# Kernel optimization log

Measured on AMD Instinct MI355X. Metric: run time of the kernel, lower is better.

Reference implementation:

```python
import jax, jax.numpy as jnp
import numpy as np
from jax import lax

# --- config matching init_kwargs ---
VOXEL_SIZE = np.array([0.25, 0.25, 8.0], np.float32)
PC_RANGE = np.array([-50.0, -50.0, -5.0, 50.0, 50.0, 3.0], np.float32)
MAX_PTS = 32
MAX_VOX = 60000
GRID = np.round((PC_RANGE[3:] - PC_RANGE[:3]) / VOXEL_SIZE).astype(np.int64)  # [400,400,1] (x,y,z)
GX, GY, GZ = int(GRID[0]), int(GRID[1]), int(GRID[2])
BIG = GX * GY * GZ  # sentinel flat id for out-of-range points
N_POINTS = 1_200_000
N_FEATS = 5


def voxelize(points):
    """points: [N, 3+C] float. Returns (out_voxels [V,P,3+C], out_coords [V,3] zyx, out_num_points [V])."""
    N = points.shape[0]
    vsize = jnp.asarray(VOXEL_SIZE)
    vmin = jnp.asarray(PC_RANGE[:3])
    # integer voxel coords per point (x,y,z)
    cxyz = jnp.floor((points[:, :3] - vmin) / vsize).astype(jnp.int32)  # [N,3]
    grid = jnp.asarray(GRID, jnp.int32)
    in_range = jnp.all((cxyz >= 0) & (cxyz < grid), axis=-1)  # [N]
    flat = cxyz[:, 2] * (GY * GX) + cxyz[:, 1] * GX + cxyz[:, 0]
    flat = jnp.where(in_range, flat, BIG)
    # stable sort by voxel id: points within a voxel keep original order (like CPU fill order)
    order = jnp.argsort(flat, stable=True)
    sf = flat[order]                      # sorted flat ids, invalid (BIG) at end
    sp = points[order]                    # [N, D]
    sc = cxyz[order]                      # [N, 3]
    ar = jnp.arange(N, dtype=jnp.int32)
    valid = sf < BIG
    new_seg = jnp.concatenate([jnp.ones((1,), bool), sf[1:] != sf[:-1]])
    first = valid & new_seg               # first point of each non-empty voxel
    vox_idx = jnp.cumsum(first.astype(jnp.int32)) - 1          # voxel slot per point
    seg_start = lax.associative_scan(jnp.maximum, jnp.where(first, ar, 0))
    rank = ar - seg_start                 # position of point within its voxel
    keep = valid & (vox_idx < MAX_VOX) & (rank < MAX_PTS)
    # out-of-bound index MAX_VOX + mode='drop' discards non-kept points
    sv = jnp.where(keep, vox_idx, MAX_VOX)
    sr = jnp.where(keep, rank, 0)
    D = points.shape[1]
    out_voxels = jnp.zeros((MAX_VOX, MAX_PTS, D), points.dtype).at[sv, sr].set(sp, mode='drop')
    out_num_points = jnp.zeros((MAX_VOX,), jnp.int32).at[sv].add(
        keep.astype(jnp.int32), mode='drop')
    coords_zyx = sc[:, ::-1]              # reorder to [z,y,x] as in the torch module
    out_coords = jnp.zeros((MAX_VOX, 3), jnp.int32).at[sv].set(coords_zyx, mode='drop')
    return out_voxels, out_coords, out_num_points


def setup_inputs() -> dict:
    key = jax.random.key(0)
    u = jax.random.uniform(key, (N_POINTS, N_FEATS), jnp.float32)
    # xyz spans slightly beyond the valid range so out-of-range masking is exercised
    lo = jnp.array([-55.0, -55.0, -6.0, 0.0, 0.0], jnp.float32)
    hi = jnp.array([55.0, 55.0, 4.0, 1.0, 1.0], jnp.float32)
    points = lo + u * (hi - lo)
    return {"points": points}


def reference(points):
    return voxelize(points)
```

## Files before the change

### kernel.cpp

```cpp
#include <hip/hip_runtime.h>


constexpr int GXc = 400;
constexpr int GYc = 400;
constexpr int NCELL = GXc * GYc;
constexpr int MAXV  = 60000;
constexpr int MAXP  = 32;
constexpr int NF    = 5;

constexpr int SCAN_B = 256;
constexpr int SCAN_E = 8;
constexpr int SCAN_TILE = SCAN_B * SCAN_E;
constexpr int NSCANBLK = (NCELL + SCAN_TILE - 1) / SCAN_TILE;

__device__ __forceinline__ int point_cell(float x, float y, float z) {
    int cx = (int)floorf((x + 50.0f) * 4.0f);
    int cy = (int)floorf((y + 50.0f) * 4.0f);
    int cz = (int)floorf((z + 5.0f) * 0.125f);
    if (cx < 0 || cx >= GXc || cy < 0 || cy >= GYc || cz != 0) return -1;
    return cy * GXc + cx;
}

__global__ void __launch_bounds__(256)
k_bin(const float* __restrict__ pts, int N,
      unsigned char* __restrict__ occupied, int* __restrict__ cellId) {
    int t = blockIdx.x * blockDim.x + threadIdx.x;
    int i0 = t * 4;
    if (i0 >= N) return;
    if (N - i0 >= 4) {
        const float4* src = (const float4*)(pts + (size_t)i0 * NF);
        float4 q0 = src[0], q1 = src[1], q2 = src[2], q3 = src[3], q4 = src[4];
        float f[20];
        *(float4*)(f + 0)  = q0; *(float4*)(f + 4)  = q1; *(float4*)(f + 8)  = q2;
        *(float4*)(f + 12) = q3; *(float4*)(f + 16) = q4;
        int cs[4];
        #pragma unroll
        for (int k = 0; k < 4; k++)
            cs[k] = point_cell(f[k * 5 + 0], f[k * 5 + 1], f[k * 5 + 2]);
        *(int4*)(cellId + i0) = make_int4(cs[0], cs[1], cs[2], cs[3]);
        #pragma unroll
        for (int k = 0; k < 4; k++)
            if (cs[k] >= 0) occupied[cs[k]] = 1;
    } else {
        for (int k = 0; k < N - i0; k++) {
            const float* p = pts + (size_t)(i0 + k) * NF;
            int c = point_cell(p[0], p[1], p[2]);
            cellId[i0 + k] = c;
            if (c >= 0) occupied[c] = 1;
        }
    }
}

__global__ void k_scanA(const unsigned char* __restrict__ occupied,
                        int* __restrict__ excl, int* __restrict__ blockSums) {
    __shared__ int sh[SCAN_B];
    int base = blockIdx.x * SCAN_TILE;
    int idx0 = base + threadIdx.x * SCAN_E;
    unsigned long long occ8 = 0;
    if (idx0 < NCELL) occ8 = *(const unsigned long long*)(occupied + idx0);
    int vals[SCAN_E];
    int sum = 0;
    #pragma unroll
    for (int e = 0; e < SCAN_E; e++) {
        int v = (int)((occ8 >> (8 * e)) & 1ull);
        vals[e] = sum;
        sum += v;
    }
    sh[threadIdx.x] = sum;
    __syncthreads();
    for (int off = 1; off < SCAN_B; off <<= 1) {
        int t = (threadIdx.x >= (unsigned)off) ? sh[threadIdx.x - off] : 0;
        __syncthreads();
        sh[threadIdx.x] += t;
        __syncthreads();
    }
    int thrExcl = (threadIdx.x == 0) ? 0 : sh[threadIdx.x - 1];
    #pragma unroll
    for (int e = 0; e < SCAN_E; e++) {
        int idx = idx0 + e;
        if (idx < NCELL) excl[idx] = thrExcl + vals[e];
    }
    if (threadIdx.x == SCAN_B - 1) blockSums[blockIdx.x] = sh[SCAN_B - 1];
}

__global__ void k_scanB(const unsigned char* __restrict__ occupied,
                        const int* __restrict__ excl,
                        const int* __restrict__ blockSums,
                        int* __restrict__ voxId,
                        int* __restrict__ cellOfVox,
                        int* __restrict__ nvoxOut) {
    __shared__ int sb[128];
    int tid = threadIdx.x;
    if (tid < 128) sb[tid] = (tid < NSCANBLK) ? blockSums[tid] : 0;
    __syncthreads();
    for (int off = 1; off < 128; off <<= 1) {
        int t = (tid < 128 && tid >= off) ? sb[tid - off] : 0;
        __syncthreads();
        if (tid < 128) sb[tid] += t;
        __syncthreads();
    }
    int c = blockIdx.x * blockDim.x + tid;
    if (c < NCELL) {
        int vi = -1;
        if (occupied[c]) {
            int blk = c / SCAN_TILE;
            int basev = (blk == 0) ? 0 : sb[blk - 1];
            int v = basev + excl[c];
            if (v < MAXV) { vi = v; cellOfVox[v] = c; }
        }
        voxId[c] = vi;
    }
    if (blockIdx.x == 0 && tid == 0) {
        int tot = sb[NSCANBLK - 1];
        *nvoxOut = tot < MAXV ? tot : MAXV;
    }
}

__global__ void __launch_bounds__(256)
k_scatter2(const int* __restrict__ cellId, int N,
           const int* __restrict__ voxId,
           int* __restrict__ vcount, int* __restrict__ slots) {
    int t = blockIdx.x * blockDim.x + threadIdx.x;
    int i0 = t * 4;
    if (i0 >= N) return;
    if (N - i0 >= 4) {
        int4 cc = *(const int4*)(cellId + i0);
        int cs[4] = {cc.x, cc.y, cc.z, cc.w};
        #pragma unroll
        for (int k = 0; k < 4; k++) {
            int c = cs[k];
            if (c >= 0) {
                int v = voxId[c];
                if (v >= 0) {
                    int pos = atomicAdd(&vcount[v], 1);
                    if (pos < MAXP) slots[v * MAXP + pos] = i0 + k;
                }
            }
        }
    } else {
        for (int k = 0; k < N - i0; k++) {
            int c = cellId[i0 + k];
            if (c >= 0) {
                int v = voxId[c];
                if (v >= 0) {
                    int pos = atomicAdd(&vcount[v], 1);
                    if (pos < MAXP) slots[v * MAXP + pos] = i0 + k;
                }
            }
        }
    }
}

__global__ void __launch_bounds__(256)
k_finalize(const float* __restrict__ pts, int N,
           const int* __restrict__ vcount,
           const int* __restrict__ slots,
           const int* __restrict__ cellOfVox,
           const int* __restrict__ nvoxPtr,
           float* __restrict__ outVox,
           float* __restrict__ outCoord,
           float* __restrict__ outNum) {
    constexpr int WV = 4;
    __shared__ float s_dat[WV][MAXP * NF];
    __shared__ int   s_key[WV][MAXP];
    __shared__ int   s_srt[WV][MAXP];

    int wv   = threadIdx.x >> 6;
    int lane = threadIdx.x & 63;
    int v    = blockIdx.x * WV + wv;
    int nvox = *nvoxPtr;

    int c = 0, num = 0;
    bool live = (v < nvox);
    if (live) {
        c = cellOfVox[v];
        int cnt = vcount[v];
        num = cnt < MAXP ? cnt : MAXP;
    }

    if (lane < MAXP)
        s_key[wv][lane] = (live && lane < num) ? slots[v * MAXP + lane] : 0x7fffffff;
    #pragma unroll
    for (int k = 0; k < 3; k++) {
        int idx = lane + 64 * k;
        if (idx < MAXP * NF) s_dat[wv][idx] = 0.0f;
    }
    __syncthreads();

    if (lane < MAXP) {
        int key = s_key[wv][lane];
        int rank = 0;
        #pragma unroll
        for (int j = 0; j < MAXP; j++) rank += (s_key[wv][j] < key) ? 1 : 0;
        if (live && lane < num) s_srt[wv][rank] = key;
    }
    __syncthreads();

    if (live && lane < num) {
        int p = s_srt[wv][lane];
        size_t byte0 = (size_t)p * 20;
        float r0, r1, r2, r3, r4, r5, r6, r7;
        int sel;
        if (byte0 + 32 <= (size_t)N * 20) {
            const float4* f4 = (const float4*)pts;
            size_t w = byte0 >> 4;
            sel = (int)((byte0 & 15) >> 2);
            float4 qa = f4[w], qb = f4[w + 1];
            r0 = qa.x; r1 = qa.y; r2 = qa.z; r3 = qa.w;
            r4 = qb.x; r5 = qb.y; r6 = qb.z; r7 = qb.w;
        } else {
            const float* s = pts + (size_t)p * NF;
            r0 = s[0]; r1 = s[1]; r2 = s[2]; r3 = s[3]; r4 = s[4];
            r5 = r6 = r7 = 0.0f; sel = 0;
        }
        float o0 = sel == 0 ? r0 : sel == 1 ? r1 : sel == 2 ? r2 : r3;
        float o1 = sel == 0 ? r1 : sel == 1 ? r2 : sel == 2 ? r3 : r4;
        float o2 = sel == 0 ? r2 : sel == 1 ? r3 : sel == 2 ? r4 : r5;
        float o3 = sel == 0 ? r3 : sel == 1 ? r4 : sel == 2 ? r5 : r6;
        float o4 = sel == 0 ? r4 : sel == 1 ? r5 : sel == 2 ? r6 : r7;
        float* d = &s_dat[wv][lane * NF];
        d[0] = o0; d[1] = o1; d[2] = o2; d[3] = o3; d[4] = o4;
    }
    __syncthreads();

    const float4* sv = (const float4*)s_dat[wv];
    float4* dst = (float4*)(outVox + (size_t)v * (MAXP * NF));
    if (lane < 40) dst[lane] = sv[lane];
    if (lane == 40) outCoord[(size_t)v * 3 + 0] = 0.0f;
    if (lane == 41) outCoord[(size_t)v * 3 + 1] = live ? (float)(c / GXc) : 0.0f;
    if (lane == 42) outCoord[(size_t)v * 3 + 2] = live ? (float)(c % GXc) : 0.0f;
    if (lane == 43) outNum[v] = live ? (float)num : 0.0f;
}

extern "C" void kernel_launch(void* const* d_in, const int* in_sizes, int n_in,
                              void* d_out, int out_size, void* d_ws, size_t ws_size,
                              hipStream_t stream) {
    const float* pts = (const float*)d_in[0];
    int N = in_sizes[0] / NF;

    float* out      = (float*)d_out;
    float* outVox   = out;
    float* outCoord = out + (size_t)MAXV * MAXP * NF;
    float* outNum   = outCoord + (size_t)MAXV * 3;

    char* ws = (char*)d_ws;
    auto take = [&](size_t bytes) {
        char* p = ws;
        ws += (bytes + 255) & ~(size_t)255;
        return p;
    };
    unsigned char* occupied = (unsigned char*)take((size_t)NCELL);
    int* vcount    = (int*)take((size_t)MAXV * 4);
    int* cellId    = (int*)take((size_t)((N + 3) & ~3) * 4);
    int* excl      = (int*)take((size_t)NCELL * 4);
    int* blockSums = (int*)take((size_t)128 * 4);
    int* voxId     = (int*)take((size_t)NCELL * 4);
    int* cellOfVox = (int*)take((size_t)MAXV * 4);
    int* slots     = (int*)take((size_t)MAXV * MAXP * 4);
    int* nvoxBuf   = (int*)take(256);

    size_t zeroBytes = (size_t)((char*)(vcount + MAXV) - (char*)occupied);
    hipMemsetAsync(occupied, 0, zeroBytes, stream);

    int nt = (N + 3) / 4;
    int nb = (nt + 255) / 256;
    k_bin<<<nb, 256, 0, stream>>>(pts, N, occupied, cellId);
    k_scanA<<<NSCANBLK, SCAN_B, 0, stream>>>(occupied, excl, blockSums);
    k_scanB<<<(NCELL + 255) / 256, 256, 0, stream>>>(occupied, excl, blockSums,
                                                     voxId, cellOfVox, nvoxBuf);
    k_scatter2<<<nb, 256, 0, stream>>>(cellId, N, voxId, vcount, slots);
    k_finalize<<<MAXV / 4, 256, 0, stream>>>(pts, N, vcount, slots, cellOfVox,
                                             nvoxBuf, outVox, outCoord, outNum);
}
```

Baseline: 129.1 us.

## Process 16 voxels per finalize block and 8 points per scatter thread

The finalize kernel now gives each wave four voxels, split into two half-wave groups of 32 lanes with two voxels per lane. This drops the block-wide __syncthreads that were only needed for wave-private shared memory and issues both voxels' point gathers before either is used, so more memory loads are in flight. The scatter kernel handles 8 points per thread and does all voxId lookups before the atomics, again to overlap loads. In exchange, fewer blocks are launched and more registers are used per thread, and correctness now depends on wave-synchronous shared-memory access without barriers.

```diff
diff --git a/kernel.cpp b/kernel.cpp
--- a/kernel.cpp
+++ b/kernel.cpp
@@ -121,20 +121,21 @@
            const int* __restrict__ voxId,
            int* __restrict__ vcount, int* __restrict__ slots) {
     int t = blockIdx.x * blockDim.x + threadIdx.x;
-    int i0 = t * 4;
+    int i0 = t * 8;
     if (i0 >= N) return;
-    if (N - i0 >= 4) {
-        int4 cc = *(const int4*)(cellId + i0);
-        int cs[4] = {cc.x, cc.y, cc.z, cc.w};
+    if (N - i0 >= 8) {
+        int4 a = *(const int4*)(cellId + i0);
+        int4 b = *(const int4*)(cellId + i0 + 4);
+        int cs[8] = {a.x, a.y, a.z, a.w, b.x, b.y, b.z, b.w};
+        int vs[8];
         #pragma unroll
-        for (int k = 0; k < 4; k++) {
-            int c = cs[k];
-            if (c >= 0) {
-                int v = voxId[c];
-                if (v >= 0) {
-                    int pos = atomicAdd(&vcount[v], 1);
-                    if (pos < MAXP) slots[v * MAXP + pos] = i0 + k;
-                }
+        for (int k = 0; k < 8; k++)
+            vs[k] = (cs[k] >= 0) ? voxId[cs[k]] : -1;
+        #pragma unroll
+        for (int k = 0; k < 8; k++) {
+            if (vs[k] >= 0) {
+                int pos = atomicAdd(&vcount[vs[k]], 1);
+                if (pos < MAXP) slots[vs[k] * MAXP + pos] = i0 + k;
             }
         }
     } else {
@@ -160,76 +161,117 @@
            float* __restrict__ outVox,
            float* __restrict__ outCoord,
            float* __restrict__ outNum) {
-    constexpr int WV = 4;
-    __shared__ float s_dat[WV][MAXP * NF];
-    __shared__ int   s_key[WV][MAXP];
-    __shared__ int   s_srt[WV][MAXP];
-
-    int wv   = threadIdx.x >> 6;
-    int lane = threadIdx.x & 63;
-    int v    = blockIdx.x * WV + wv;
+    __shared__ int   s_key[4][4][MAXP];
+    __shared__ int   s_srt[4][4][MAXP];
+    __shared__ float s_dat[4][4][MAXP * NF];
+
+    int tid  = threadIdx.x;
+    int wv   = tid >> 6, lane = tid & 63;
+    int h    = lane >> 5, s = lane & 31;
+    int vb   = (blockIdx.x * 4 + wv) * 4;
     int nvox = *nvoxPtr;
 
-    int c = 0, num = 0;
-    bool live = (v < nvox);
-    if (live) {
-        c = cellOfVox[v];
-        int cnt = vcount[v];
-        num = cnt < MAXP ? cnt : MAXP;
-    }
-
-    if (lane < MAXP)
-        s_key[wv][lane] = (live && lane < num) ? slots[v * MAXP + lane] : 0x7fffffff;
-    #pragma unroll
-    for (int k = 0; k < 3; k++) {
-        int idx = lane + 64 * k;
-        if (idx < MAXP * NF) s_dat[wv][idx] = 0.0f;
-    }
-    __syncthreads();
-
-    if (lane < MAXP) {
-        int key = s_key[wv][lane];
-        int rank = 0;
-        #pragma unroll
-        for (int j = 0; j < MAXP; j++) rank += (s_key[wv][j] < key) ? 1 : 0;
-        if (live && lane < num) s_srt[wv][rank] = key;
-    }
-    __syncthreads();
-
-    if (live && lane < num) {
-        int p = s_srt[wv][lane];
-        size_t byte0 = (size_t)p * 20;
+    int u0 = vb + h, u1 = vb + 2 + h;
+    bool live0 = u0 < nvox, live1 = u1 < nvox;
+    int num0 = 0, num1 = 0;
+    if (live0) { int cnt = vcount[u0]; num0 = cnt < MAXP ? cnt : MAXP; }
+    if (live1) { int cnt = vcount[u1]; num1 = cnt < MAXP ? cnt : MAXP; }
+
+    int k0 = (live0 && s < num0) ? slots[u0 * MAXP + s] : 0x7fffffff;
+    int k1 = (live1 && s < num1) ? slots[u1 * MAXP + s] : 0x7fffffff;
+    s_key[wv][h][s]     = k0;
+    s_key[wv][2 + h][s] = k1;
+
+    float* flat = (float*)s_dat[wv];
+    #pragma unroll
+    for (int q = 0; q < 10; q++) flat[q * 64 + lane] = 0.0f;
+
+    int rank0 = 0, rank1 = 0;
+    #pragma unroll
+    for (int j = 0; j < MAXP; j++) rank0 += (s_key[wv][h][j] < k0) ? 1 : 0;
+    #pragma unroll
+    for (int j = 0; j < MAXP; j++) rank1 += (s_key[wv][2 + h][j] < k1) ? 1 : 0;
+    bool g0 = live0 && s < num0, g1 = live1 && s < num1;
+    if (g0) s_srt[wv][h][rank0]     = k0;
+    if (g1) s_srt[wv][2 + h][rank1] = k1;
+
+    int p0 = g0 ? s_srt[wv][h][s]     : 0;
+    int p1 = g1 ? s_srt[wv][2 + h][s] : 0;
+    float4 qa0, qb0, qa1, qb1;
+    int sel0 = -1, sel1 = -1;
+    size_t lim = (size_t)N * 20;
+    const float4* f4 = (const float4*)pts;
+    if (g0) {
+        size_t b = (size_t)p0 * 20;
+        if (b + 32 <= lim) {
+            sel0 = (int)((b & 15) >> 2);
+            size_t w = b >> 4;
+            qa0 = f4[w]; qb0 = f4[w + 1];
+        }
+    }
+    if (g1) {
+        size_t b = (size_t)p1 * 20;
+        if (b + 32 <= lim) {
+            sel1 = (int)((b & 15) >> 2);
+            size_t w = b >> 4;
+            qa1 = f4[w]; qb1 = f4[w + 1];
+        }
+    }
+    if (g0) {
         float r0, r1, r2, r3, r4, r5, r6, r7;
-        int sel;
-        if (byte0 + 32 <= (size_t)N * 20) {
-            const float4* f4 = (const float4*)pts;
-            size_t w = byte0 >> 4;
-            sel = (int)((byte0 & 15) >> 2);
-            float4 qa = f4[w], qb = f4[w + 1];
-            r0 = qa.x; r1 = qa.y; r2 = qa.z; r3 = qa.w;
-            r4 = qb.x; r5 = qb.y; r6 = qb.z; r7 = qb.w;
+        if (sel0 >= 0) {
+            r0 = qa0.x; r1 = qa0.y; r2 = qa0.z; r3 = qa0.w;
+            r4 = qb0.x; r5 = qb0.y; r6 = qb0.z; r7 = qb0.w;
         } else {
-            const float* s = pts + (size_t)p * NF;
-            r0 = s[0]; r1 = s[1]; r2 = s[2]; r3 = s[3]; r4 = s[4];
-            r5 = r6 = r7 = 0.0f; sel = 0;
-        }
-        float o0 = sel == 0 ? r0 : sel == 1 ? r1 : sel == 2 ? r2 : r3;
-        float o1 = sel == 0 ? r1 : sel == 1 ? r2 : sel == 2 ? r3 : r4;
-        float o2 = sel == 0 ? r2 : sel == 1 ? r3 : sel == 2 ? r4 : r5;
-        float o3 = sel == 0 ? r3 : sel == 1 ? r4 : sel == 2 ? r5 : r6;
-        float o4 = sel == 0 ? r4 : sel == 1 ? r5 : sel == 2 ? r6 : r7;
-        float* d = &s_dat[wv][lane * NF];
+            const float* sp = pts + (size_t)p0 * NF;
+            r0 = sp[0]; r1 = sp[1]; r2 = sp[2]; r3 = sp[3]; r4 = sp[4];
+            r5 = r6 = r7 = 0.0f; sel0 = 0;
+        }
+        float o0 = sel0 == 0 ? r0 : sel0 == 1 ? r1 : sel0 == 2 ? r2 : r3;
+        float o1 = sel0 == 0 ? r1 : sel0 == 1 ? r2 : sel0 == 2 ? r3 : r4;
+        float o2 = sel0 == 0 ? r2 : sel0 == 1 ? r3 : sel0 == 2 ? r4 : r5;
+        float o3 = sel0 == 0 ? r3 : sel0 == 1 ? r4 : sel0 == 2 ? r5 : r6;
+        float o4 = sel0 == 0 ? r4 : sel0 == 1 ? r5 : sel0 == 2 ? r6 : r7;
+        float* d = &s_dat[wv][h][s * NF];
         d[0] = o0; d[1] = o1; d[2] = o2; d[3] = o3; d[4] = o4;
     }
-    __syncthreads();
+    if (g1) {
+        float r0, r1, r2, r3, r4, r5, r6, r7;
+        if (sel1 >= 0) {
+            r0 = qa1.x; r1 = qa1.y; r2 = qa1.z; r3 = qa1.w;
+            r4 = qb1.x; r5 = qb1.y; r6 = qb1.z; r7 = qb1.w;
+        } else {
+            const float* sp = pts + (size_t)p1 * NF;
+            r0 = sp[0]; r1 = sp[1]; r2 = sp[2]; r3 = sp[3]; r4 = sp[4];
+            r5 = r6 = r7 = 0.0f; sel1 = 0;
+        }
+        float o0 = sel1 == 0 ? r0 : sel1 == 1 ? r1 : sel1 == 2 ? r2 : r3;
+        float o1 = sel1 == 0 ? r1 : sel1 == 1 ? r2 : sel1 == 2 ? r3 : r4;
+        float o2 = sel1 == 0 ? r2 : sel1 == 1 ? r3 : sel1 == 2 ? r4 : r5;
+        float o3 = sel1 == 0 ? r3 : sel1 == 1 ? r4 : sel1 == 2 ? r5 : r6;
+        float o4 = sel1 == 0 ? r4 : sel1 == 1 ? r5 : sel1 == 2 ? r6 : r7;
+        float* d = &s_dat[wv][2 + h][s * NF];
+        d[0] = o0; d[1] = o1; d[2] = o2; d[3] = o3; d[4] = o4;
+    }
 
     const float4* sv = (const float4*)s_dat[wv];
-    float4* dst = (float4*)(outVox + (size_t)v * (MAXP * NF));
-    if (lane < 40) dst[lane] = sv[lane];
-    if (lane == 40) outCoord[(size_t)v * 3 + 0] = 0.0f;
-    if (lane == 41) outCoord[(size_t)v * 3 + 1] = live ? (float)(c / GXc) : 0.0f;
-    if (lane == 42) outCoord[(size_t)v * 3 + 2] = live ? (float)(c % GXc) : 0.0f;
-    if (lane == 43) outNum[v] = live ? (float)num : 0.0f;
+    float4* dst = (float4*)(outVox + (size_t)vb * (MAXP * NF));
+    #pragma unroll
+    for (int q = 0; q < 3; q++) {
+        int idx = q * 64 + lane;
+        if (idx < 160) dst[idx] = sv[idx];
+    }
+    if (lane < 4) {
+        int v = vb + lane;
+        bool lv = v < nvox;
+        int c = lv ? cellOfVox[v] : 0;
+        int cnt = lv ? vcount[v] : 0;
+        int num = cnt < MAXP ? cnt : MAXP;
+        outNum[v] = lv ? (float)num : 0.0f;
+        outCoord[(size_t)v * 3 + 0] = 0.0f;
+        outCoord[(size_t)v * 3 + 1] = lv ? (float)(c / GXc) : 0.0f;
+        outCoord[(size_t)v * 3 + 2] = lv ? (float)(c % GXc) : 0.0f;
+    }
 }
 
 extern "C" void kernel_launch(void* const* d_in, const int* in_sizes, int n_in,
@@ -251,7 +293,7 @@
     };
     unsigned char* occupied = (unsigned char*)take((size_t)NCELL);
     int* vcount    = (int*)take((size_t)MAXV * 4);
-    int* cellId    = (int*)take((size_t)((N + 3) & ~3) * 4);
+    int* cellId    = (int*)take((size_t)((N + 7) & ~7) * 4);
     int* excl      = (int*)take((size_t)NCELL * 4);
     int* blockSums = (int*)take((size_t)128 * 4);
     int* voxId     = (int*)take((size_t)NCELL * 4);
@@ -262,13 +304,13 @@
     size_t zeroBytes = (size_t)((char*)(vcount + MAXV) - (char*)occupied);
     hipMemsetAsync(occupied, 0, zeroBytes, stream);
 
-    int nt = (N + 3) / 4;
-    int nb = (nt + 255) / 256;
-    k_bin<<<nb, 256, 0, stream>>>(pts, N, occupied, cellId);
+    int nb4 = ((N + 3) / 4 + 255) / 256;
+    k_bin<<<nb4, 256, 0, stream>>>(pts, N, occupied, cellId);
     k_scanA<<<NSCANBLK, SCAN_B, 0, stream>>>(occupied, excl, blockSums);
     k_scanB<<<(NCELL + 255) / 256, 256, 0, stream>>>(occupied, excl, blockSums,
                                                      voxId, cellOfVox, nvoxBuf);
-    k_scatter2<<<nb, 256, 0, stream>>>(cellId, N, voxId, vcount, slots);
-    k_finalize<<<MAXV / 4, 256, 0, stream>>>(pts, N, vcount, slots, cellOfVox,
-                                             nvoxBuf, outVox, outCoord, outNum);
-}
+    int nb8 = ((N + 7) / 8 + 255) / 256;
+    k_scatter2<<<nb8, 256, 0, stream>>>(cellId, N, voxId, vcount, slots);
+    k_finalize<<<MAXV / 16, 256, 0, stream>>>(pts, N, vcount, slots, cellOfVox,
+                                              nvoxBuf, outVox, outCoord, outNum);
+}
```

After: 120.7 us. 6.5% less time.
